# Kernel optimization log

Hardware: AMD Instinct MI355X
Metric: run time of the kernel (lower is better)

The kernel has to match this reference:

```python
import jax, jax.numpy as jnp
import numpy as np


def reference(x, weight, bias):
    """Per-sample dynamic conv2d, expressed as one grouped convolution.

    x:      (B, C_in, H, W)
    weight: (B, C_out, C_in, kH, kW)
    bias:   (B, C_out)
    returns (B, C_out, H_out, W_out) with H_out = H - kH + 1 (valid conv)
    """
    B, C_in, H, W = x.shape
    C_out, kH, kW = weight.shape[1], weight.shape[3], weight.shape[4]
    # Fold batch into channels: groups=B grouped conv == B independent convs.
    x_g = x.reshape(1, B * C_in, H, W)
    w_g = weight.reshape(B * C_out, C_in, kH, kW)
    out = jax.lax.conv_general_dilated(
        x_g, w_g,
        window_strides=(1, 1),
        padding='VALID',
        dimension_numbers=('NCHW', 'OIHW', 'NCHW'),
        feature_group_count=B,
    )  # (1, B*C_out, H_out, W_out)
    out = out.reshape(B, C_out, out.shape[2], out.shape[3])
    return out + bias[:, :, None, None]


def setup_inputs() -> dict:
    key = jax.random.key(0)
    k1, k2, k3 = jax.random.split(key, 3)
    B, C_in, C_out, H, W, kH, kW = 16, 64, 64, 128, 128, 3, 3
    x = jax.random.normal(k1, (B, C_in, H, W), dtype=jnp.float32)
    weight = jax.random.normal(k2, (B, C_out, C_in, kH, kW), dtype=jnp.float32) * 0.05
    bias = jax.random.normal(k3, (B, C_out), dtype=jnp.float32)
    return {"x": x, "weight": weight, "bias": bias}
```

## Files before the change

kernel.cpp:

```cpp
#include <hip/hip_runtime.h>

#define BATCH 16
#define CI 64
#define CO 64
#define H 128
#define W 128
#define HO 126
#define WO 126

typedef short bfrag __attribute__((ext_vector_type(8)));
typedef float ffrag __attribute__((ext_vector_type(4)));

static __device__ __forceinline__ unsigned short f2bf(float f) {
    unsigned u = __float_as_uint(f);
    u += 0x7fffu + ((u >> 16) & 1u);
    return (unsigned short)(u >> 16);
}

__global__ void wt_prepass(const float* __restrict__ w, unsigned short* __restrict__ w_t) {
    int i = blockIdx.x * 256 + threadIdx.x;
    int ci = i & 63;
    int co = (i >> 6) & 63;
    int bs = i >> 12;
    int b = bs / 9, s = bs - b * 9;
    w_t[i] = f2bf(w[(((b * 64 + co) * 64 + ci) * 9) + s]);
}

static __device__ __forceinline__ int xchunk(int row, int col, int o) {
    return ((row << 7) + col) * 8 + (o ^ (col & 7) ^ ((row & 1) << 2));
}

__launch_bounds__(256, 2)
__global__ void dynconv_mfma(const float* __restrict__ x,
                             const unsigned short* __restrict__ w_t,
                             const float* __restrict__ bias,
                             float* __restrict__ out) {
    __shared__ __align__(16) unsigned short x_t[4 * 128 * 64];
    __shared__ __align__(16) unsigned short A_lds[64 * 64];

    const int tid = threadIdx.x;
    const int rg  = blockIdx.x;
    const int b   = blockIdx.y;
    const int y0  = rg * 2;

    const int wave = tid >> 6;
    const int lane = tid & 63;
    const int l16  = lane & 15;
    const int lq   = lane >> 4;
    const int wm   = wave & 1;
    const int wn   = wave >> 1;

    {
        const float* xb = x + (size_t)b * CI * H * W;
        #pragma unroll
        for (int it = 0; it < 16; ++it) {
            int item = it * 256 + tid;
            int colq = item & 31;
            int row  = (item >> 5) & 3;
            int cp   = item >> 7;
            const float* p = xb + ((size_t)(2 * cp) * H + (y0 + row)) * W + colq * 4;
            float4 f0 = *(const float4*)p;
            float4 f1 = *(const float4*)(p + H * W);
            int o = cp >> 2;
            int e = (2 * cp) & 7;
            #pragma unroll
            for (int jj = 0; jj < 4; ++jj) {
                int j = (jj + colq) & 3;
                int col = colq * 4 + j;
                float a0 = (&f0.x)[j], a1 = (&f1.x)[j];
                *(unsigned int*)&x_t[xchunk(row, col, o) * 8 + e] =
                    (unsigned int)f2bf(a0) | ((unsigned int)f2bf(a1) << 16);
            }
        }
    }

    ffrag acc[2][8];
    #pragma unroll
    for (int mt = 0; mt < 2; ++mt)
        #pragma unroll
        for (int nt = 0; nt < 8; ++nt)
            acc[mt][nt] = (ffrag){0.f, 0.f, 0.f, 0.f};

    const bfrag* gw = (const bfrag*)w_t + (size_t)(b * 9) * 512;
    bfrag w0 = gw[2 * tid];
    bfrag w1 = gw[2 * tid + 1];

    for (int s = 0; s < 9; ++s) {
        const int dy = s / 3, dx = s - dy * 3;
        __syncthreads();
        {
            int co_s = tid >> 2;
            int o0 = (tid & 3) * 2;
            *(bfrag*)&A_lds[(co_s * 8 + (o0 ^ (co_s & 7))) * 8] = w0;
            *(bfrag*)&A_lds[(co_s * 8 + ((o0 + 1) ^ (co_s & 7))) * 8] = w1;
        }
        if (s < 8) {
            w0 = gw[(s + 1) * 512 + 2 * tid];
            w1 = gw[(s + 1) * 512 + 2 * tid + 1];
        }
        __syncthreads();

        const int xr = wn + dy;
        #pragma unroll
        for (int ks = 0; ks < 2; ++ks) {
            const int o = ks * 4 + lq;
            bfrag a0, a1;
            {
                int co_a = wm * 32 + l16;
                a0 = *(const bfrag*)&A_lds[(co_a * 8 + (o ^ (co_a & 7))) * 8];
                co_a += 16;
                a1 = *(const bfrag*)&A_lds[(co_a * 8 + (o ^ (co_a & 7))) * 8];
            }
            #pragma unroll
            for (int nt = 0; nt < 8; ++nt) {
                int colx = nt * 16 + l16 + dx;
                if (colx > 127) colx = 127;
                bfrag bf = *(const bfrag*)&x_t[xchunk(xr, colx, o) * 8];
                acc[0][nt] = __builtin_amdgcn_mfma_f32_16x16x32_bf16(a0, bf, acc[0][nt], 0, 0, 0);
                acc[1][nt] = __builtin_amdgcn_mfma_f32_16x16x32_bf16(a1, bf, acc[1][nt], 0, 0, 0);
            }
        }
    }

    const int oy = y0 + wn;
    #pragma unroll
    for (int mt = 0; mt < 2; ++mt) {
        #pragma unroll
        for (int r = 0; r < 4; ++r) {
            int co = wm * 32 + mt * 16 + lq * 4 + r;
            float bv = bias[b * 64 + co];
            float* op = out + ((size_t)(b * 64 + co) * HO + oy) * WO;
            #pragma unroll
            for (int nt = 0; nt < 8; ++nt) {
                int ox = nt * 16 + l16;
                if (ox < WO) op[ox] = acc[mt][nt][r] + bv;
            }
        }
    }
}

extern "C" void kernel_launch(void* const* d_in, const int* in_sizes, int n_in,
                              void* d_out, int out_size, void* d_ws, size_t ws_size,
                              hipStream_t stream) {
    const float* x    = (const float*)d_in[0];
    const float* w    = (const float*)d_in[1];
    const float* bias = (const float*)d_in[2];
    float* out        = (float*)d_out;
    unsigned short* w_t = (unsigned short*)d_ws;

    wt_prepass<<<dim3(589824 / 256), dim3(256), 0, stream>>>(w, w_t);
    dynconv_mfma<<<dim3(63, BATCH), dim3(256), 0, stream>>>(x, w_t, bias, out);
}
```

Baseline: 159.1 us.

## Pre-transpose x to bf16 in a prepass and stream it via global_load_lds

```diff
diff --git a/kernel.cpp b/kernel.cpp
--- a/kernel.cpp
+++ b/kernel.cpp
@@ -10,6 +10,9 @@
 
 typedef short bfrag __attribute__((ext_vector_type(8)));
 typedef float ffrag __attribute__((ext_vector_type(4)));
+
+#define AS3(p) ((__attribute__((address_space(3))) void*)(p))
+#define AS1(p) ((const __attribute__((address_space(1))) void*)(p))
 
 static __device__ __forceinline__ unsigned short f2bf(float f) {
     unsigned u = __float_as_uint(f);
@@ -26,23 +29,52 @@
     w_t[i] = f2bf(w[(((b * 64 + co) * 64 + ci) * 9) + s]);
 }
 
-static __device__ __forceinline__ int xchunk(int row, int col, int o) {
-    return ((row << 7) + col) * 8 + (o ^ (col & 7) ^ ((row & 1) << 2));
+__global__ void xt_prepass(const float* __restrict__ x, unsigned short* __restrict__ x_tg) {
+    __shared__ float tile[64 * 32 * 4];
+    const int tid = threadIdx.x;
+    const int y = blockIdx.x;
+    const int b = blockIdx.y;
+
+    const float* xp = x + (size_t)b * CI * H * W + (size_t)y * W;
+    #pragma unroll
+    for (int p = 0; p < 8; ++p) {
+        int item = p * 256 + tid;
+        int colq = item & 31;
+        int ci   = item >> 5;
+        float4 v = *(const float4*)(xp + (size_t)ci * H * W + colq * 4);
+        int slot = colq ^ (ci >> 3);
+        *(float4*)&tile[(ci * 32 + slot) * 4] = v;
+    }
+    __syncthreads();
+
+    unsigned short* og = x_tg + ((size_t)(b * 128 + y)) * 1024 * 8;
+    #pragma unroll
+    for (int q = 0; q < 4; ++q) {
+        int item = q * 256 + tid;
+        int o   = item & 7;
+        int col = item >> 3;
+        unsigned short u[8];
+        #pragma unroll
+        for (int e = 0; e < 8; ++e) {
+            int ci = o * 8 + e;
+            u[e] = f2bf(tile[(ci * 32 + ((col >> 2) ^ o)) * 4 + (col & 3)]);
+        }
+        int chunk = col * 8 + (o ^ (col & 7));
+        *(uint4*)&og[chunk * 8] = *(const uint4*)u;
+    }
 }
 
 __launch_bounds__(256, 2)
-__global__ void dynconv_mfma(const float* __restrict__ x,
+__global__ void dynconv_mfma(const unsigned short* __restrict__ x_tg,
                              const unsigned short* __restrict__ w_t,
                              const float* __restrict__ bias,
                              float* __restrict__ out) {
-    __shared__ __align__(16) unsigned short x_t[4 * 128 * 64];
-    __shared__ __align__(16) unsigned short A_lds[64 * 64];
+    __shared__ __align__(16) unsigned short xs[4 * 8192];
 
-    const int tid = threadIdx.x;
-    const int rg  = blockIdx.x;
-    const int b   = blockIdx.y;
-    const int y0  = rg * 2;
-
+    const int tid  = threadIdx.x;
+    const int rg   = blockIdx.x;
+    const int b    = blockIdx.y;
+    const int y0   = rg * 2;
     const int wave = tid >> 6;
     const int lane = tid & 63;
     const int l16  = lane & 15;
@@ -51,28 +83,23 @@
     const int wn   = wave >> 1;
 
     {
-        const float* xb = x + (size_t)b * CI * H * W;
+        const unsigned short* gsrc = x_tg + ((size_t)(b * 128 + y0 + wave)) * 8192;
         #pragma unroll
-        for (int it = 0; it < 16; ++it) {
-            int item = it * 256 + tid;
-            int colq = item & 31;
-            int row  = (item >> 5) & 3;
-            int cp   = item >> 7;
-            const float* p = xb + ((size_t)(2 * cp) * H + (y0 + row)) * W + colq * 4;
-            float4 f0 = *(const float4*)p;
-            float4 f1 = *(const float4*)(p + H * W);
-            int o = cp >> 2;
-            int e = (2 * cp) & 7;
-            #pragma unroll
-            for (int jj = 0; jj < 4; ++jj) {
-                int j = (jj + colq) & 3;
-                int col = colq * 4 + j;
-                float a0 = (&f0.x)[j], a1 = (&f1.x)[j];
-                *(unsigned int*)&x_t[xchunk(row, col, o) * 8 + e] =
-                    (unsigned int)f2bf(a0) | ((unsigned int)f2bf(a1) << 16);
-            }
+        for (int i = 0; i < 16; ++i) {
+            __builtin_amdgcn_global_load_lds(AS1(gsrc + i * 512 + lane * 8),
+                                             AS3(xs + wave * 8192 + i * 512),
+                                             16, 0, 0);
         }
     }
+
+    const bfrag* wtb = (const bfrag*)w_t + (size_t)(b * 9) * 512;
+    const int co_b = wm * 32 + l16;
+    bfrag acur[4], anxt[4];
+    #pragma unroll
+    for (int ks = 0; ks < 2; ++ks)
+        #pragma unroll
+        for (int mt = 0; mt < 2; ++mt)
+            acur[ks * 2 + mt] = wtb[(co_b + mt * 16) * 8 + ks * 4 + lq];
 
     ffrag acc[2][8];
     #pragma unroll
@@ -81,45 +108,33 @@
         for (int nt = 0; nt < 8; ++nt)
             acc[mt][nt] = (ffrag){0.f, 0.f, 0.f, 0.f};
 
-    const bfrag* gw = (const bfrag*)w_t + (size_t)(b * 9) * 512;
-    bfrag w0 = gw[2 * tid];
-    bfrag w1 = gw[2 * tid + 1];
+    __syncthreads();
 
     for (int s = 0; s < 9; ++s) {
+        if (s < 8) {
+            const bfrag* wn2 = wtb + (s + 1) * 512;
+            #pragma unroll
+            for (int ks = 0; ks < 2; ++ks)
+                #pragma unroll
+                for (int mt = 0; mt < 2; ++mt)
+                    anxt[ks * 2 + mt] = wn2[(co_b + mt * 16) * 8 + ks * 4 + lq];
+        }
         const int dy = s / 3, dx = s - dy * 3;
-        __syncthreads();
-        {
-            int co_s = tid >> 2;
-            int o0 = (tid & 3) * 2;
-            *(bfrag*)&A_lds[(co_s * 8 + (o0 ^ (co_s & 7))) * 8] = w0;
-            *(bfrag*)&A_lds[(co_s * 8 + ((o0 + 1) ^ (co_s & 7))) * 8] = w1;
-        }
-        if (s < 8) {
-            w0 = gw[(s + 1) * 512 + 2 * tid];
-            w1 = gw[(s + 1) * 512 + 2 * tid + 1];
-        }
-        __syncthreads();
-
         const int xr = wn + dy;
         #pragma unroll
         for (int ks = 0; ks < 2; ++ks) {
             const int o = ks * 4 + lq;
-            bfrag a0, a1;
-            {
-                int co_a = wm * 32 + l16;
-                a0 = *(const bfrag*)&A_lds[(co_a * 8 + (o ^ (co_a & 7))) * 8];
-                co_a += 16;
-                a1 = *(const bfrag*)&A_lds[(co_a * 8 + (o ^ (co_a & 7))) * 8];
-            }
             #pragma unroll
             for (int nt = 0; nt < 8; ++nt) {
                 int colx = nt * 16 + l16 + dx;
                 if (colx > 127) colx = 127;
-                bfrag bf = *(const bfrag*)&x_t[xchunk(xr, colx, o) * 8];
-                acc[0][nt] = __builtin_amdgcn_mfma_f32_16x16x32_bf16(a0, bf, acc[0][nt], 0, 0, 0);
-                acc[1][nt] = __builtin_amdgcn_mfma_f32_16x16x32_bf16(a1, bf, acc[1][nt], 0, 0, 0);
+                const bfrag bf = *(const bfrag*)&xs[xr * 8192 + (colx * 8 + (o ^ (colx & 7))) * 8];
+                acc[0][nt] = __builtin_amdgcn_mfma_f32_16x16x32_bf16(acur[ks * 2 + 0], bf, acc[0][nt], 0, 0, 0);
+                acc[1][nt] = __builtin_amdgcn_mfma_f32_16x16x32_bf16(acur[ks * 2 + 1], bf, acc[1][nt], 0, 0, 0);
             }
         }
+        #pragma unroll
+        for (int j = 0; j < 4; ++j) acur[j] = anxt[j];
     }
 
     const int oy = y0 + wn;
@@ -146,8 +161,11 @@
     const float* w    = (const float*)d_in[1];
     const float* bias = (const float*)d_in[2];
     float* out        = (float*)d_out;
-    unsigned short* w_t = (unsigned short*)d_ws;
+
+    unsigned short* w_t  = (unsigned short*)d_ws;
+    unsigned short* x_tg = (unsigned short*)((char*)d_ws + 1179648);
 
     wt_prepass<<<dim3(589824 / 256), dim3(256), 0, stream>>>(w, w_t);
-    dynconv_mfma<<<dim3(63, BATCH), dim3(256), 0, stream>>>(x, w_t, bias, out);
+    xt_prepass<<<dim3(128, BATCH), dim3(256), 0, stream>>>(x, x_tg);
+    dynconv_mfma<<<dim3(63, BATCH), dim3(256), 0, stream>>>(x_tg, w_t, bias, out);
 }
```

Measured after the change: 151.9 us. 4.6% less time.
